# Kernel optimization log

Measured on AMD Instinct MI355X. Metric: run time of the kernel, lower is better.

The kernel has to match this reference:

```python
import jax, jax.numpy as jnp
import numpy as np

N = 100000
E = 1600000


def gcn_conv(x, W, b, src, dst, dinv):
    # PyG GCNConv: h = x @ W; symmetric normalization with self-loops;
    # out[i] = sum_{j->i} dinv[j]*dinv[i]*h[j] + dinv[i]^2*h[i] + b
    h = x @ W
    norm = dinv[src] * dinv[dst]                      # [E]
    msg = h[src] * norm[:, None]                      # [E, d] gather
    out = jax.ops.segment_sum(msg, dst, num_segments=N)  # scatter-add
    out = out + h * (dinv * dinv)[:, None]            # self-loop term
    return out + b


def setup_inputs() -> dict:
    key = jax.random.key(0)
    ks = jax.random.split(key, 8)
    nfeat, nhid, nclass = 128, 128, 40
    x = jax.random.normal(ks[0], (N, nfeat), dtype=jnp.float32)
    edge_index = jax.random.randint(ks[1], (2, E), 0, N, dtype=jnp.int64)
    s = 1.0 / np.sqrt(nfeat)
    W0 = jax.random.uniform(ks[2], (nfeat, nhid), jnp.float32, -s, s)
    b0 = jnp.zeros((nhid,), jnp.float32)
    W1 = jax.random.uniform(ks[3], (nhid, nhid), jnp.float32, -s, s)
    b1 = jnp.zeros((nhid,), jnp.float32)
    W2 = jax.random.uniform(ks[4], (nhid, nclass), jnp.float32, -s, s)
    b2 = jnp.zeros((nclass,), jnp.float32)
    return {"x": x, "W0": W0, "b0": b0, "W1": W1, "b1": b1,
            "W2": W2, "b2": b2, "edge_index": edge_index}


def reference(x, W0, b0, W1, b1, W2, b2, edge_index):
    src, dst = edge_index[0], edge_index[1]
    # degree (with self-loop) on destination nodes, symmetric norm
    deg = jax.ops.segment_sum(jnp.ones((E,), jnp.float32), dst, num_segments=N) + 1.0
    dinv = jax.lax.rsqrt(deg)
    h = gcn_conv(x, W0, b0, src, dst, dinv)
    h = jax.nn.relu(h)  # dropout is identity in eval mode
    h = gcn_conv(h, W1, b1, src, dst, dinv)
    h = jax.nn.relu(h)
    out = gcn_conv(h, W2, b2, src, dst, dinv)
    return out
```

## Files before the change

kernel.cpp:

```cpp
#include <hip/hip_runtime.h>
#include <hip/hip_fp16.h>


#define CAP 8192
#define NBMAX 512

typedef _Float16 f16;
typedef __attribute__((ext_vector_type(8))) _Float16 f16x8;
typedef __attribute__((ext_vector_type(4))) _Float16 f16x4;
typedef __attribute__((ext_vector_type(4))) float f32x4;

__global__ __launch_bounds__(256)
void bucket_prep_kernel(const int* __restrict__ src, const int* __restrict__ dst,
                        int E, int gP1, int NB,
                        int* __restrict__ bucket_cnt, unsigned* __restrict__ bucketbuf,
                        const float* __restrict__ W0, const float* __restrict__ W1,
                        const float* __restrict__ W2,
                        __half* __restrict__ w0t, __half* __restrict__ w1t,
                        __half* __restrict__ w2t) {
  int b = blockIdx.x;
  if (b < gP1) {
    __shared__ int hist[NBMAX];
    __shared__ int cbase[NBMAX];
    int tid = threadIdx.x;
    for (int i = tid; i < NB; i += 256) hist[i] = 0;
    __syncthreads();
    int e0 = b * 4096;
    int eend = min(e0 + 4096, E);
    for (int e = e0 + tid; e < eend; e += 256)
      atomicAdd(&hist[((unsigned)dst[e]) >> 8], 1);
    __syncthreads();
    for (int i = tid; i < NB; i += 256) {
      int h = hist[i];
      cbase[i] = h ? atomicAdd(&bucket_cnt[i], h) : 0;
    }
    __syncthreads();
    for (int i = tid; i < NB; i += 256) hist[i] = 0;
    __syncthreads();
    for (int e = e0 + tid; e < eend; e += 256) {
      int d = dst[e];
      int s = src[e];
      int bk = ((unsigned)d) >> 8;
      int idx = cbase[bk] + atomicAdd(&hist[bk], 1);
      if (idx < CAP)
        bucketbuf[(size_t)bk * CAP + idx] = (((unsigned)s) << 8) | (unsigned)(d & 255);
    }
  } else {
    int i = (b - gP1) * 256 + threadIdx.x;
    if (i < 16384) {
      int n = i >> 7, k = i & 127;
      w0t[i] = __float2half_rn(W0[k * 128 + n]);
    } else if (i < 32768) {
      int j = i - 16384;
      int n = j >> 7, k = j & 127;
      w1t[j] = __float2half_rn(W1[k * 128 + n]);
    } else if (i < 38912) {
      int j = i - 32768;
      int n = j >> 7, k = j & 127;
      w2t[j] = (n < 40) ? __float2half_rn(W2[k * 40 + n]) : __float2half_rn(0.f);
    }
  }
}

struct P2Shared {
  unsigned plist[CAP];
  int cnts[256];
  int sm[256];
};

__device__ __forceinline__
void phase2_body(const unsigned* __restrict__ bucketbuf, const int* __restrict__ bucket_cnt,
                 int* __restrict__ rowptr, float* __restrict__ dinv,
                 int* __restrict__ col, int N, int E, int NB, int b, P2Shared& sh) {
  int tid = threadIdx.x;
  int cnt_b = min(bucket_cnt[b], CAP);

  int part = 0;
  for (int i = tid; i < b; i += 256) part += bucket_cnt[i];
  sh.sm[tid] = part;
  __syncthreads();
#pragma unroll
  for (int off = 128; off > 0; off >>= 1) {
    if (tid < off) sh.sm[tid] += sh.sm[tid + off];
    __syncthreads();
  }
  int base = sh.sm[0];
  __syncthreads();

  for (int i = tid; i < cnt_b; i += 256)
    sh.plist[i] = bucketbuf[(size_t)b * CAP + i];
  sh.cnts[tid] = 0;
  __syncthreads();
  for (int i = tid; i < cnt_b; i += 256)
    atomicAdd(&sh.cnts[sh.plist[i] & 255u], 1);
  __syncthreads();

  int myc = sh.cnts[tid];
  sh.sm[tid] = myc;
  __syncthreads();
#pragma unroll
  for (int off = 1; off < 256; off <<= 1) {
    int u = (tid >= off) ? sh.sm[tid - off] : 0;
    __syncthreads();
    sh.sm[tid] += u;
    __syncthreads();
  }
  int exc = sh.sm[tid] - myc;

  int n = (b << 8) + tid;
  if (n < N) {
    rowptr[n] = base + exc;
    dinv[n] = 1.0f / sqrtf((float)myc + 1.0f);
  }
  if (b == NB - 1 && tid == 0) rowptr[N] = E;
  __syncthreads();

  sh.cnts[tid] = base + exc;
  __syncthreads();
  for (int i = tid; i < cnt_b; i += 256) {
    unsigned p = sh.plist[i];
    int pos = atomicAdd(&sh.cnts[p & 255u], 1);
    col[pos] = (int)(p >> 8);
  }
}

template <typename TIN, bool SCALE>
__device__ __forceinline__
void mfma_gemm128_body(const TIN* __restrict__ X, const __half* __restrict__ Wt,
                       const float* __restrict__ dinv, __half* __restrict__ G,
                       int nrows, int blk, f16 (*xs)[72], f16 (*ws)[72]) {
  const int tid = threadIdx.x;
  const int wave = tid >> 6;
  const int lane = tid & 63;
  const int mrow = lane & 15;
  const int kg = lane >> 4;
  const int row0 = blk * 128;

  f32x4 acc[2][8];
#pragma unroll
  for (int i = 0; i < 2; ++i)
#pragma unroll
    for (int j = 0; j < 8; ++j) acc[i][j] = (f32x4){0.f, 0.f, 0.f, 0.f};

  for (int k0 = 0; k0 < 128; k0 += 64) {
    if constexpr (sizeof(TIN) == 4) {
#pragma unroll
      for (int t = tid; t < 2048; t += 256) {
        int r = t >> 4;
        int kk = (t & 15) * 4;
        float4 v = make_float4(0.f, 0.f, 0.f, 0.f);
        if (row0 + r < nrows)
          v = *(const float4*)((const float*)X + (size_t)(row0 + r) * 128 + k0 + kk);
        f16x4 hv = {(f16)v.x, (f16)v.y, (f16)v.z, (f16)v.w};
        *(f16x4*)&xs[r][kk] = hv;
      }
    } else {
#pragma unroll
      for (int t = tid; t < 1024; t += 256) {
        int r = t >> 3;
        int kk = (t & 7) * 8;
        f16x8 v = (f16x8){0, 0, 0, 0, 0, 0, 0, 0};
        if (row0 + r < nrows)
          v = *(const f16x8*)((const f16*)X + (size_t)(row0 + r) * 128 + k0 + kk);
        *(f16x8*)&xs[r][kk] = v;
      }
    }
#pragma unroll
    for (int t = tid; t < 1024; t += 256) {
      int r = t >> 3;
      int kk = (t & 7) * 8;
      *(f16x8*)&ws[r][kk] =
          *(const f16x8*)((const f16*)Wt + (size_t)r * 128 + k0 + kk);
    }
    __syncthreads();
#pragma unroll
    for (int ks = 0; ks < 64; ks += 32) {
      f16x8 a0 = *(const f16x8*)&xs[wave * 32 + mrow][ks + kg * 8];
      f16x8 a1 = *(const f16x8*)&xs[wave * 32 + 16 + mrow][ks + kg * 8];
#pragma unroll
      for (int nt = 0; nt < 8; ++nt) {
        f16x8 b = *(const f16x8*)&ws[nt * 16 + mrow][ks + kg * 8];
        acc[0][nt] = __builtin_amdgcn_mfma_f32_16x16x32_f16(a0, b, acc[0][nt], 0, 0, 0);
        acc[1][nt] = __builtin_amdgcn_mfma_f32_16x16x32_f16(a1, b, acc[1][nt], 0, 0, 0);
      }
    }
    __syncthreads();
  }
#pragma unroll
  for (int mt = 0; mt < 2; ++mt) {
    int rbase = row0 + wave * 32 + mt * 16 + kg * 4;
#pragma unroll
    for (int i = 0; i < 4; ++i) {
      int grow = rbase + i;
      if (grow < nrows) {
        float s = SCALE ? dinv[grow] : 1.0f;
        __half* gp = G + (size_t)grow * 128 + mrow;
#pragma unroll
        for (int nt = 0; nt < 8; ++nt)
          gp[nt * 16] = __float2half_rn(s * acc[mt][nt][i]);
      }
    }
  }
}

__global__ __launch_bounds__(256)
void mfma_gemm128_kernel(const __half* __restrict__ X, const __half* __restrict__ Wt,
                         const float* __restrict__ dinv, __half* __restrict__ G,
                         int nrows) {
  __shared__ f16 xs[128][72];
  __shared__ f16 ws[128][72];
  mfma_gemm128_body<__half, true>(X, Wt, dinv, G, nrows, blockIdx.x, xs, ws);
}

__global__ __launch_bounds__(256)
void gemm128_build_kernel(const float* __restrict__ X, const __half* __restrict__ Wt,
                          __half* __restrict__ G, int nrows, int gGemm,
                          const unsigned* __restrict__ bucketbuf,
                          const int* __restrict__ bucket_cnt,
                          int* __restrict__ rowptr, float* __restrict__ dinv,
                          int* __restrict__ col, int N, int E, int NB) {
  __shared__ char shraw[2 * 128 * 72 * sizeof(f16)];
  if ((int)blockIdx.x < gGemm) {
    f16 (*xs)[72] = (f16(*)[72])shraw;
    f16 (*ws)[72] = (f16(*)[72])(shraw + 128 * 72 * sizeof(f16));
    mfma_gemm128_body<float, false>(X, Wt, nullptr, G, nrows, blockIdx.x, xs, ws);
  } else {
    phase2_body(bucketbuf, bucket_cnt, rowptr, dinv, col, N, E, NB,
                blockIdx.x - gGemm, *(P2Shared*)shraw);
  }
}

__global__ __launch_bounds__(256)
void mfma_gemm48_kernel(const __half* __restrict__ X, const __half* __restrict__ Wt,
                        const float* __restrict__ dinv, __half* __restrict__ G,
                        int nrows) {
  __shared__ f16 xs[128][72];
  __shared__ f16 ws[48][72];
  const int tid = threadIdx.x;
  const int wave = tid >> 6;
  const int lane = tid & 63;
  const int mrow = lane & 15;
  const int kg = lane >> 4;
  const int row0 = blockIdx.x * 128;

  f32x4 acc[2][3];
#pragma unroll
  for (int i = 0; i < 2; ++i)
#pragma unroll
    for (int j = 0; j < 3; ++j) acc[i][j] = (f32x4){0.f, 0.f, 0.f, 0.f};

  for (int k0 = 0; k0 < 128; k0 += 64) {
#pragma unroll
    for (int t = tid; t < 1024; t += 256) {
      int r = t >> 3;
      int kk = (t & 7) * 8;
      f16x8 v = (f16x8){0, 0, 0, 0, 0, 0, 0, 0};
      if (row0 + r < nrows)
        v = *(const f16x8*)((const f16*)X + (size_t)(row0 + r) * 128 + k0 + kk);
      *(f16x8*)&xs[r][kk] = v;
    }
#pragma unroll
    for (int t = tid; t < 384; t += 256) {
      int r = t >> 3;
      int kk = (t & 7) * 8;
      *(f16x8*)&ws[r][kk] =
          *(const f16x8*)((const f16*)Wt + (size_t)r * 128 + k0 + kk);
    }
    __syncthreads();
#pragma unroll
    for (int ks = 0; ks < 64; ks += 32) {
      f16x8 a0 = *(const f16x8*)&xs[wave * 32 + mrow][ks + kg * 8];
      f16x8 a1 = *(const f16x8*)&xs[wave * 32 + 16 + mrow][ks + kg * 8];
#pragma unroll
      for (int nt = 0; nt < 3; ++nt) {
        f16x8 b = *(const f16x8*)&ws[nt * 16 + mrow][ks + kg * 8];
        acc[0][nt] = __builtin_amdgcn_mfma_f32_16x16x32_f16(a0, b, acc[0][nt], 0, 0, 0);
        acc[1][nt] = __builtin_amdgcn_mfma_f32_16x16x32_f16(a1, b, acc[1][nt], 0, 0, 0);
      }
    }
    __syncthreads();
  }
#pragma unroll
  for (int mt = 0; mt < 2; ++mt) {
    int rbase = row0 + wave * 32 + mt * 16 + kg * 4;
#pragma unroll
    for (int i = 0; i < 4; ++i) {
      int grow = rbase + i;
      if (grow < nrows) {
        float s = dinv[grow];
#pragma unroll
        for (int nt = 0; nt < 3; ++nt) {
          int c = nt * 16 + mrow;
          if (c < 40)
            G[(size_t)grow * 40 + c] = __float2half_rn(s * acc[mt][nt][i]);
        }
      }
    }
  }
}

template <bool RELU, bool WEIGHTED, typename TOUT>
__global__ __launch_bounds__(256)
void aggregate128_kernel(const __half* __restrict__ G, const int* __restrict__ rowptr,
                         const int* __restrict__ col, const float* __restrict__ dinv,
                         const float* __restrict__ bias, TOUT* __restrict__ out,
                         int n, int Em1) {
  int wid = threadIdx.x >> 6;
  int lane = threadIdx.x & 63;
  int node = blockIdx.x * 4 + wid;
  if (node >= n) return;

  int sub = lane >> 4;
  int c = lane & 15;
  const float4* g4 = (const float4*)G;

  int e = rowptr[node];
  int end = rowptr[node + 1];
  float di = dinv[node];

  float a0 = 0.f, a1 = 0.f, a2 = 0.f, a3 = 0.f,
        a4 = 0.f, a5 = 0.f, a6 = 0.f, a7 = 0.f;

  auto accumw = [&](float4 raw, float w) {
    const __half2* h = (const __half2*)&raw;
    float2 f0 = __half22float2(h[0]);
    float2 f1 = __half22float2(h[1]);
    float2 f2 = __half22float2(h[2]);
    float2 f3 = __half22float2(h[3]);
    a0 = fmaf(w, f0.x, a0); a1 = fmaf(w, f0.y, a1);
    a2 = fmaf(w, f1.x, a2); a3 = fmaf(w, f1.y, a3);
    a4 = fmaf(w, f2.x, a4); a5 = fmaf(w, f2.y, a5);
    a6 = fmaf(w, f3.x, a6); a7 = fmaf(w, f3.y, a7);
  };

  if (sub == 0)
    accumw(g4[(size_t)node * 16 + c], WEIGHTED ? di : 1.0f);

  int base = e;
  int i0 = base + sub * 4;
  int s0 = col[min(i0, Em1)];
  int s1 = col[min(i0 + 1, Em1)];
  int s2 = col[min(i0 + 2, Em1)];
  int s3 = col[min(i0 + 3, Em1)];

  while (base < end) {
    int ii = base + sub * 4;
    float4 z = make_float4(0.f, 0.f, 0.f, 0.f);
    float4 r0 = z, r1 = z, r2 = z, r3 = z;
    if (ii < end)     r0 = g4[(size_t)s0 * 16 + c];
    if (ii + 1 < end) r1 = g4[(size_t)s1 * 16 + c];
    if (ii + 2 < end) r2 = g4[(size_t)s2 * 16 + c];
    if (ii + 3 < end) r3 = g4[(size_t)s3 * 16 + c];
    float w0 = 1.f, w1 = 1.f, w2 = 1.f, w3 = 1.f;
    if (WEIGHTED) { w0 = dinv[s0]; w1 = dinv[s1]; w2 = dinv[s2]; w3 = dinv[s3]; }
    base += 16;
    int ni = base + sub * 4;
    int t0 = col[min(ni, Em1)];
    int t1 = col[min(ni + 1, Em1)];
    int t2 = col[min(ni + 2, Em1)];
    int t3 = col[min(ni + 3, Em1)];
    accumw(r0, w0);
    accumw(r1, w1);
    accumw(r2, w2);
    accumw(r3, w3);
    s0 = t0; s1 = t1; s2 = t2; s3 = t3;
  }

  a0 += __shfl_xor(a0, 16); a1 += __shfl_xor(a1, 16);
  a2 += __shfl_xor(a2, 16); a3 += __shfl_xor(a3, 16);
  a4 += __shfl_xor(a4, 16); a5 += __shfl_xor(a5, 16);
  a6 += __shfl_xor(a6, 16); a7 += __shfl_xor(a7, 16);
  a0 += __shfl_xor(a0, 32); a1 += __shfl_xor(a1, 32);
  a2 += __shfl_xor(a2, 32); a3 += __shfl_xor(a3, 32);
  a4 += __shfl_xor(a4, 32); a5 += __shfl_xor(a5, 32);
  a6 += __shfl_xor(a6, 32); a7 += __shfl_xor(a7, 32);

  if (sub == 0) {
    const float4* b4 = (const float4*)bias;
    float4 bb0 = b4[c * 2];
    float4 bb1 = b4[c * 2 + 1];
    float o[8] = {di * a0 + bb0.x, di * a1 + bb0.y, di * a2 + bb0.z,
                  di * a3 + bb0.w, di * a4 + bb1.x, di * a5 + bb1.y,
                  di * a6 + bb1.z, di * a7 + bb1.w};
    if (RELU) {
#pragma unroll
      for (int j = 0; j < 8; ++j) o[j] = fmaxf(o[j], 0.f);
    }
    if constexpr (sizeof(TOUT) == 2) {
      union { __half2 h[4]; float4 f; } u;
      u.h[0] = __floats2half2_rn(o[0], o[1]);
      u.h[1] = __floats2half2_rn(o[2], o[3]);
      u.h[2] = __floats2half2_rn(o[4], o[5]);
      u.h[3] = __floats2half2_rn(o[6], o[7]);
      *(float4*)((__half*)out + (size_t)node * 128 + c * 8) = u.f;
    } else {
      float4* op = (float4*)((float*)out + (size_t)node * 128 + c * 8);
      op[0] = make_float4(o[0], o[1], o[2], o[3]);
      op[1] = make_float4(o[4], o[5], o[6], o[7]);
    }
  }
}

__global__ __launch_bounds__(256)
void aggregate40_kernel(const __half* __restrict__ G, const int* __restrict__ rowptr,
                        const int* __restrict__ col, const float* __restrict__ dinv,
                        const float* __restrict__ bias, float* __restrict__ out,
                        int n, int Em1) {
  int wid = threadIdx.x >> 6;
  int lane = threadIdx.x & 63;
  int node = blockIdx.x * 4 + wid;
  if (node >= n) return;

  int sub = lane / 10;
  int c = lane % 10;
  bool act = sub < 6;
  const float2* g2 = (const float2*)G;

  int e = rowptr[node];
  int end = rowptr[node + 1];
  float di = dinv[node];

  float ax = 0.f, ay = 0.f, az = 0.f, aw = 0.f;
  auto acc2 = [&](float2 raw) {
    float2 f0 = __half22float2(*(const __half2*)&raw.x);
    float2 f1 = __half22float2(*(const __half2*)&raw.y);
    ax += f0.x; ay += f0.y; az += f1.x; aw += f1.y;
  };
  if (lane < 10) acc2(g2[(size_t)node * 10 + c]);

  int base = e;
  int i0 = base + sub * 2;
  int s0 = col[min(i0, Em1)];
  int s1 = col[min(i0 + 1, Em1)];

  while (base < end) {
    int ii = base + sub * 2;
    float2 z = make_float2(0.f, 0.f);
    float2 r0 = z, r1 = z;
    if (act && ii < end)     r0 = g2[(size_t)s0 * 10 + c];
    if (act && ii + 1 < end) r1 = g2[(size_t)s1 * 10 + c];
    base += 12;
    int ni = base + sub * 2;
    int t0 = col[min(ni, Em1)];
    int t1 = col[min(ni + 1, Em1)];
    acc2(r0);
    acc2(r1);
    s0 = t0; s1 = t1;
  }

  float bx = __shfl(ax, lane + 30), by = __shfl(ay, lane + 30),
        bz = __shfl(az, lane + 30), bw = __shfl(aw, lane + 30);
  ax += bx; ay += by; az += bz; aw += bw;
  float c1x = __shfl(ax, lane + 10), c1y = __shfl(ay, lane + 10),
        c1z = __shfl(az, lane + 10), c1w = __shfl(aw, lane + 10);
  float c2x = __shfl(ax, lane + 20), c2y = __shfl(ay, lane + 20),
        c2z = __shfl(az, lane + 20), c2w = __shfl(aw, lane + 20);

  if (lane < 10) {
    float sx = ax + c1x + c2x;
    float sy = ay + c1y + c2y;
    float sz = az + c1z + c2z;
    float sw = aw + c1w + c2w;
    float4 bb = ((const float4*)bias)[c];
    float4 o = make_float4(di * sx + bb.x, di * sy + bb.y, di * sz + bb.z,
                           di * sw + bb.w);
    ((float4*)out)[(size_t)node * 10 + c] = o;
  }
}

extern "C" void kernel_launch(void* const* d_in, const int* in_sizes, int n_in,
                              void* d_out, int out_size, void* d_ws, size_t ws_size,
                              hipStream_t stream) {
  const float* x = (const float*)d_in[0];
  const float* W0 = (const float*)d_in[1];
  const float* b0 = (const float*)d_in[2];
  const float* W1 = (const float*)d_in[3];
  const float* b1 = (const float*)d_in[4];
  const float* W2 = (const float*)d_in[5];
  const float* b2 = (const float*)d_in[6];
  const int* ei = (const int*)d_in[7];

  const int N = in_sizes[0] / 128;
  const int E = in_sizes[7] / 2;
  const int* src = ei;
  const int* dst = ei + E;
  const int NB = (N + 255) >> 8;

  char* w = (char*)d_ws;
  size_t off = 0;
  auto alloc = [&](size_t bytes) -> void* {
    void* p = w + off;
    off = (off + bytes + 255) & ~(size_t)255;
    return p;
  };
  int* bucket_cnt = (int*)alloc((size_t)NBMAX * 4);
  float* dinv = (float*)alloc((size_t)N * 4);
  int* rowptr = (int*)alloc((size_t)(N + 1) * 4);
  int* col = (int*)alloc((size_t)E * 4);
  unsigned* bucketbuf = (unsigned*)alloc((size_t)NB * CAP * 4);
  __half* gbuf = (__half*)alloc((size_t)N * 128 * 2);
  __half* hbuf = (__half*)alloc((size_t)N * 128 * 2);
  __half* w0t = (__half*)alloc(128 * 128 * 2);
  __half* w1t = (__half*)alloc(128 * 128 * 2);
  __half* w2t = (__half*)alloc(48 * 128 * 2);
  (void)ws_size;

  hipMemsetAsync(bucket_cnt, 0, (size_t)NBMAX * 4, stream);

  dim3 blk(256);
  int gP1 = (E + 4095) / 4096;
  int gW = (38912 + 255) / 256;
  int gGemm = (N + 127) / 128;
  int gAgg = (N + 3) / 4;

  bucket_prep_kernel<<<gP1 + gW, blk, 0, stream>>>(src, dst, E, gP1, NB,
                                                   bucket_cnt, bucketbuf,
                                                   W0, W1, W2, w0t, w1t, w2t);
  gemm128_build_kernel<<<gGemm + NB, blk, 0, stream>>>(x, w0t, gbuf, N, gGemm,
                                                       bucketbuf, bucket_cnt,
                                                       rowptr, dinv, col, N, E, NB);

  aggregate128_kernel<true, true, __half><<<gAgg, blk, 0, stream>>>(
      gbuf, rowptr, col, dinv, b0, hbuf, N, E - 1);
  mfma_gemm128_kernel<<<gGemm, blk, 0, stream>>>(hbuf, w1t, dinv, gbuf, N);
  aggregate128_kernel<true, false, __half><<<gAgg, blk, 0, stream>>>(
      gbuf, rowptr, col, dinv, b1, hbuf, N, E - 1);
  mfma_gemm48_kernel<<<gGemm, blk, 0, stream>>>(hbuf, w2t, dinv, gbuf, N);
  aggregate40_kernel<<<gAgg, blk, 0, stream>>>(gbuf, rowptr, col, dinv, b2,
                                               (float*)d_out, N, E - 1);
}
```

Measured before the change: 365.0 us.

## Process four nodes per wave with software-pipelined column-index prefetch in aggregation

Each wavefront in the aggregation kernels now handles four consecutive nodes instead of one. While gathering the current node's neighbors, it prefetches the next node's rowptr and column indices. The first 20 (or 24) edges are gathered unconditionally with zeroed weights for out-of-range slots, and a tail loop handles the rest. This hides index-load latency and amortizes launch and wave setup, at the cost of fewer waves in flight and some wasted gathers for low-degree nodes.

```diff
diff --git a/kernel.cpp b/kernel.cpp
--- a/kernel.cpp
+++ b/kernel.cpp
@@ -304,100 +304,124 @@
 void aggregate128_kernel(const __half* __restrict__ G, const int* __restrict__ rowptr,
                          const int* __restrict__ col, const float* __restrict__ dinv,
                          const float* __restrict__ bias, TOUT* __restrict__ out,
-                         int n, int Em1) {
+                         int n) {
+  constexpr int NPW = 4;
   int wid = threadIdx.x >> 6;
   int lane = threadIdx.x & 63;
-  int node = blockIdx.x * 4 + wid;
-  if (node >= n) return;
+  int n0 = (blockIdx.x * 4 + wid) * NPW;
+  if (n0 >= n) return;
 
   int sub = lane >> 4;
   int c = lane & 15;
   const float4* g4 = (const float4*)G;
 
-  int e = rowptr[node];
-  int end = rowptr[node + 1];
-  float di = dinv[node];
-
-  float a0 = 0.f, a1 = 0.f, a2 = 0.f, a3 = 0.f,
-        a4 = 0.f, a5 = 0.f, a6 = 0.f, a7 = 0.f;
-
-  auto accumw = [&](float4 raw, float w) {
-    const __half2* h = (const __half2*)&raw;
-    float2 f0 = __half22float2(h[0]);
-    float2 f1 = __half22float2(h[1]);
-    float2 f2 = __half22float2(h[2]);
-    float2 f3 = __half22float2(h[3]);
-    a0 = fmaf(w, f0.x, a0); a1 = fmaf(w, f0.y, a1);
-    a2 = fmaf(w, f1.x, a2); a3 = fmaf(w, f1.y, a3);
-    a4 = fmaf(w, f2.x, a4); a5 = fmaf(w, f2.y, a5);
-    a6 = fmaf(w, f3.x, a6); a7 = fmaf(w, f3.y, a7);
-  };
-
-  if (sub == 0)
-    accumw(g4[(size_t)node * 16 + c], WEIGHTED ? di : 1.0f);
-
-  int base = e;
-  int i0 = base + sub * 4;
-  int s0 = col[min(i0, Em1)];
-  int s1 = col[min(i0 + 1, Em1)];
-  int s2 = col[min(i0 + 2, Em1)];
-  int s3 = col[min(i0 + 3, Em1)];
-
-  while (base < end) {
-    int ii = base + sub * 4;
-    float4 z = make_float4(0.f, 0.f, 0.f, 0.f);
-    float4 r0 = z, r1 = z, r2 = z, r3 = z;
-    if (ii < end)     r0 = g4[(size_t)s0 * 16 + c];
-    if (ii + 1 < end) r1 = g4[(size_t)s1 * 16 + c];
-    if (ii + 2 < end) r2 = g4[(size_t)s2 * 16 + c];
-    if (ii + 3 < end) r3 = g4[(size_t)s3 * 16 + c];
-    float w0 = 1.f, w1 = 1.f, w2 = 1.f, w3 = 1.f;
-    if (WEIGHTED) { w0 = dinv[s0]; w1 = dinv[s1]; w2 = dinv[s2]; w3 = dinv[s3]; }
-    base += 16;
-    int ni = base + sub * 4;
-    int t0 = col[min(ni, Em1)];
-    int t1 = col[min(ni + 1, Em1)];
-    int t2 = col[min(ni + 2, Em1)];
-    int t3 = col[min(ni + 3, Em1)];
-    accumw(r0, w0);
-    accumw(r1, w1);
-    accumw(r2, w2);
-    accumw(r3, w3);
-    s0 = t0; s1 = t1; s2 = t2; s3 = t3;
-  }
-
-  a0 += __shfl_xor(a0, 16); a1 += __shfl_xor(a1, 16);
-  a2 += __shfl_xor(a2, 16); a3 += __shfl_xor(a3, 16);
-  a4 += __shfl_xor(a4, 16); a5 += __shfl_xor(a5, 16);
-  a6 += __shfl_xor(a6, 16); a7 += __shfl_xor(a7, 16);
-  a0 += __shfl_xor(a0, 32); a1 += __shfl_xor(a1, 32);
-  a2 += __shfl_xor(a2, 32); a3 += __shfl_xor(a3, 32);
-  a4 += __shfl_xor(a4, 32); a5 += __shfl_xor(a5, 32);
-  a6 += __shfl_xor(a6, 32); a7 += __shfl_xor(a7, 32);
-
-  if (sub == 0) {
-    const float4* b4 = (const float4*)bias;
-    float4 bb0 = b4[c * 2];
-    float4 bb1 = b4[c * 2 + 1];
-    float o[8] = {di * a0 + bb0.x, di * a1 + bb0.y, di * a2 + bb0.z,
-                  di * a3 + bb0.w, di * a4 + bb1.x, di * a5 + bb1.y,
-                  di * a6 + bb1.z, di * a7 + bb1.w};
-    if (RELU) {
-#pragma unroll
-      for (int j = 0; j < 8; ++j) o[j] = fmaxf(o[j], 0.f);
-    }
-    if constexpr (sizeof(TOUT) == 2) {
-      union { __half2 h[4]; float4 f; } u;
-      u.h[0] = __floats2half2_rn(o[0], o[1]);
-      u.h[1] = __floats2half2_rn(o[2], o[3]);
-      u.h[2] = __floats2half2_rn(o[4], o[5]);
-      u.h[3] = __floats2half2_rn(o[6], o[7]);
-      *(float4*)((__half*)out + (size_t)node * 128 + c * 8) = u.f;
-    } else {
-      float4* op = (float4*)((float*)out + (size_t)node * 128 + c * 8);
-      op[0] = make_float4(o[0], o[1], o[2], o[3]);
-      op[1] = make_float4(o[4], o[5], o[6], o[7]);
-    }
+  int eA = rowptr[n0], endA = rowptr[n0 + 1];
+  int n1 = min(n0 + 1, n - 1);
+  int eB = rowptr[n1], endB = rowptr[n1 + 1];
+
+  int lastA = (endA > eA) ? endA - 1 : 0;
+  int iA = eA + sub;
+  int cA0 = col[min(iA,      lastA)];
+  int cA1 = col[min(iA + 4,  lastA)];
+  int cA2 = col[min(iA + 8,  lastA)];
+  int cA3 = col[min(iA + 12, lastA)];
+  int cA4 = col[min(iA + 16, lastA)];
+
+#pragma unroll
+  for (int j = 0; j < NPW; ++j) {
+    int node = n0 + j;
+    if (node >= n) break;
+
+    float4 r0 = g4[(size_t)cA0 * 16 + c];
+    float4 r1 = g4[(size_t)cA1 * 16 + c];
+    float4 r2 = g4[(size_t)cA2 * 16 + c];
+    float4 r3 = g4[(size_t)cA3 * 16 + c];
+    float4 r4 = g4[(size_t)cA4 * 16 + c];
+    float4 rs = g4[(size_t)node * 16 + c];
+    float dv0 = 1.f, dv1 = 1.f, dv2 = 1.f, dv3 = 1.f, dv4 = 1.f;
+    if (WEIGHTED) {
+      dv0 = dinv[cA0]; dv1 = dinv[cA1]; dv2 = dinv[cA2];
+      dv3 = dinv[cA3]; dv4 = dinv[cA4];
+    }
+    float di = dinv[node];
+
+    int n2 = min(node + 2, n - 1);
+    int eC = rowptr[n2];
+    int endC = rowptr[n2 + 1];
+
+    int lastB = (endB > eB) ? endB - 1 : 0;
+    int iB = eB + sub;
+    int cB0 = col[min(iB,      lastB)];
+    int cB1 = col[min(iB + 4,  lastB)];
+    int cB2 = col[min(iB + 8,  lastB)];
+    int cB3 = col[min(iB + 12, lastB)];
+    int cB4 = col[min(iB + 16, lastB)];
+
+    float a0 = 0.f, a1 = 0.f, a2 = 0.f, a3 = 0.f,
+          a4 = 0.f, a5 = 0.f, a6 = 0.f, a7 = 0.f;
+    auto accumw = [&](float4 raw, float w) {
+      const __half2* h = (const __half2*)&raw;
+      float2 f0 = __half22float2(h[0]);
+      float2 f1 = __half22float2(h[1]);
+      float2 f2 = __half22float2(h[2]);
+      float2 f3 = __half22float2(h[3]);
+      a0 = fmaf(w, f0.x, a0); a1 = fmaf(w, f0.y, a1);
+      a2 = fmaf(w, f1.x, a2); a3 = fmaf(w, f1.y, a3);
+      a4 = fmaf(w, f2.x, a4); a5 = fmaf(w, f2.y, a5);
+      a6 = fmaf(w, f3.x, a6); a7 = fmaf(w, f3.y, a7);
+    };
+    accumw(rs, (sub == 0) ? (WEIGHTED ? di : 1.f) : 0.f);
+    accumw(r0, (iA      < endA) ? dv0 : 0.f);
+    accumw(r1, (iA + 4  < endA) ? dv1 : 0.f);
+    accumw(r2, (iA + 8  < endA) ? dv2 : 0.f);
+    accumw(r3, (iA + 12 < endA) ? dv3 : 0.f);
+    accumw(r4, (iA + 16 < endA) ? dv4 : 0.f);
+
+    for (int t = eA + 20; t < endA; t += 4) {
+      int it = t + sub;
+      if (it < endA) {
+        int sc = col[it];
+        accumw(g4[(size_t)sc * 16 + c], WEIGHTED ? dinv[sc] : 1.f);
+      }
+    }
+
+    a0 += __shfl_xor(a0, 16); a1 += __shfl_xor(a1, 16);
+    a2 += __shfl_xor(a2, 16); a3 += __shfl_xor(a3, 16);
+    a4 += __shfl_xor(a4, 16); a5 += __shfl_xor(a5, 16);
+    a6 += __shfl_xor(a6, 16); a7 += __shfl_xor(a7, 16);
+    a0 += __shfl_xor(a0, 32); a1 += __shfl_xor(a1, 32);
+    a2 += __shfl_xor(a2, 32); a3 += __shfl_xor(a3, 32);
+    a4 += __shfl_xor(a4, 32); a5 += __shfl_xor(a5, 32);
+    a6 += __shfl_xor(a6, 32); a7 += __shfl_xor(a7, 32);
+
+    if (sub == 0) {
+      const float4* b4 = (const float4*)bias;
+      float4 bb0 = b4[c * 2];
+      float4 bb1 = b4[c * 2 + 1];
+      float o[8] = {di * a0 + bb0.x, di * a1 + bb0.y, di * a2 + bb0.z,
+                    di * a3 + bb0.w, di * a4 + bb1.x, di * a5 + bb1.y,
+                    di * a6 + bb1.z, di * a7 + bb1.w};
+      if (RELU) {
+#pragma unroll
+        for (int k = 0; k < 8; ++k) o[k] = fmaxf(o[k], 0.f);
+      }
+      if constexpr (sizeof(TOUT) == 2) {
+        union { __half2 h[4]; float4 f; } u;
+        u.h[0] = __floats2half2_rn(o[0], o[1]);
+        u.h[1] = __floats2half2_rn(o[2], o[3]);
+        u.h[2] = __floats2half2_rn(o[4], o[5]);
+        u.h[3] = __floats2half2_rn(o[6], o[7]);
+        *(float4*)((__half*)out + (size_t)node * 128 + c * 8) = u.f;
+      } else {
+        float4* op = (float4*)((float*)out + (size_t)node * 128 + c * 8);
+        op[0] = make_float4(o[0], o[1], o[2], o[3]);
+        op[1] = make_float4(o[4], o[5], o[6], o[7]);
+      }
+    }
+
+    eA = eB; endA = endB; eB = eC; endB = endC;
+    iA = eA + sub;
+    cA0 = cB0; cA1 = cB1; cA2 = cB2; cA3 = cB3; cA4 = cB4;
   }
 }
 
@@ -405,66 +429,95 @@
 void aggregate40_kernel(const __half* __restrict__ G, const int* __restrict__ rowptr,
                         const int* __restrict__ col, const float* __restrict__ dinv,
                         const float* __restrict__ bias, float* __restrict__ out,
-                        int n, int Em1) {
+                        int n) {
+  constexpr int NPW = 4;
   int wid = threadIdx.x >> 6;
   int lane = threadIdx.x & 63;
-  int node = blockIdx.x * 4 + wid;
-  if (node >= n) return;
+  int n0 = (blockIdx.x * 4 + wid) * NPW;
+  if (n0 >= n) return;
 
   int sub = lane / 10;
   int c = lane % 10;
   bool act = sub < 6;
   const float2* g2 = (const float2*)G;
 
-  int e = rowptr[node];
-  int end = rowptr[node + 1];
-  float di = dinv[node];
-
-  float ax = 0.f, ay = 0.f, az = 0.f, aw = 0.f;
-  auto acc2 = [&](float2 raw) {
-    float2 f0 = __half22float2(*(const __half2*)&raw.x);
-    float2 f1 = __half22float2(*(const __half2*)&raw.y);
-    ax += f0.x; ay += f0.y; az += f1.x; aw += f1.y;
-  };
-  if (lane < 10) acc2(g2[(size_t)node * 10 + c]);
-
-  int base = e;
-  int i0 = base + sub * 2;
-  int s0 = col[min(i0, Em1)];
-  int s1 = col[min(i0 + 1, Em1)];
-
-  while (base < end) {
-    int ii = base + sub * 2;
-    float2 z = make_float2(0.f, 0.f);
-    float2 r0 = z, r1 = z;
-    if (act && ii < end)     r0 = g2[(size_t)s0 * 10 + c];
-    if (act && ii + 1 < end) r1 = g2[(size_t)s1 * 10 + c];
-    base += 12;
-    int ni = base + sub * 2;
-    int t0 = col[min(ni, Em1)];
-    int t1 = col[min(ni + 1, Em1)];
-    acc2(r0);
-    acc2(r1);
-    s0 = t0; s1 = t1;
-  }
-
-  float bx = __shfl(ax, lane + 30), by = __shfl(ay, lane + 30),
-        bz = __shfl(az, lane + 30), bw = __shfl(aw, lane + 30);
-  ax += bx; ay += by; az += bz; aw += bw;
-  float c1x = __shfl(ax, lane + 10), c1y = __shfl(ay, lane + 10),
-        c1z = __shfl(az, lane + 10), c1w = __shfl(aw, lane + 10);
-  float c2x = __shfl(ax, lane + 20), c2y = __shfl(ay, lane + 20),
-        c2z = __shfl(az, lane + 20), c2w = __shfl(aw, lane + 20);
-
-  if (lane < 10) {
-    float sx = ax + c1x + c2x;
-    float sy = ay + c1y + c2y;
-    float sz = az + c1z + c2z;
-    float sw = aw + c1w + c2w;
-    float4 bb = ((const float4*)bias)[c];
-    float4 o = make_float4(di * sx + bb.x, di * sy + bb.y, di * sz + bb.z,
-                           di * sw + bb.w);
-    ((float4*)out)[(size_t)node * 10 + c] = o;
+  int eA = rowptr[n0], endA = rowptr[n0 + 1];
+  int n1 = min(n0 + 1, n - 1);
+  int eB = rowptr[n1], endB = rowptr[n1 + 1];
+
+  int lastA = (endA > eA) ? endA - 1 : 0;
+  int iA = eA + sub * 4;
+  int cA0 = col[min(iA,     lastA)];
+  int cA1 = col[min(iA + 1, lastA)];
+  int cA2 = col[min(iA + 2, lastA)];
+  int cA3 = col[min(iA + 3, lastA)];
+
+#pragma unroll
+  for (int j = 0; j < NPW; ++j) {
+    int node = n0 + j;
+    if (node >= n) break;
+
+    float2 r0 = g2[(size_t)cA0 * 10 + c];
+    float2 r1 = g2[(size_t)cA1 * 10 + c];
+    float2 r2 = g2[(size_t)cA2 * 10 + c];
+    float2 r3 = g2[(size_t)cA3 * 10 + c];
+    float2 rs = g2[(size_t)node * 10 + c];
+    float di = dinv[node];
+
+    int n2 = min(node + 2, n - 1);
+    int eC = rowptr[n2];
+    int endC = rowptr[n2 + 1];
+
+    int lastB = (endB > eB) ? endB - 1 : 0;
+    int iB = eB + sub * 4;
+    int cB0 = col[min(iB,     lastB)];
+    int cB1 = col[min(iB + 1, lastB)];
+    int cB2 = col[min(iB + 2, lastB)];
+    int cB3 = col[min(iB + 3, lastB)];
+
+    float ax = 0.f, ay = 0.f, az = 0.f, aw = 0.f;
+    auto acc2w = [&](float2 raw, float w) {
+      float2 f0 = __half22float2(*(const __half2*)&raw.x);
+      float2 f1 = __half22float2(*(const __half2*)&raw.y);
+      ax = fmaf(w, f0.x, ax); ay = fmaf(w, f0.y, ay);
+      az = fmaf(w, f1.x, az); aw = fmaf(w, f1.y, aw);
+    };
+    acc2w(rs, (lane < 10) ? 1.f : 0.f);
+    acc2w(r0, (act && iA     < endA) ? 1.f : 0.f);
+    acc2w(r1, (act && iA + 1 < endA) ? 1.f : 0.f);
+    acc2w(r2, (act && iA + 2 < endA) ? 1.f : 0.f);
+    acc2w(r3, (act && iA + 3 < endA) ? 1.f : 0.f);
+
+    for (int t = eA + 24; t < endA; t += 6) {
+      int it = t + sub;
+      if (act && it < endA) {
+        int sc = col[it];
+        acc2w(g2[(size_t)sc * 10 + c], 1.f);
+      }
+    }
+
+    float bx = __shfl(ax, lane + 30), by = __shfl(ay, lane + 30),
+          bz = __shfl(az, lane + 30), bw = __shfl(aw, lane + 30);
+    ax += bx; ay += by; az += bz; aw += bw;
+    float c1x = __shfl(ax, lane + 10), c1y = __shfl(ay, lane + 10),
+          c1z = __shfl(az, lane + 10), c1w = __shfl(aw, lane + 10);
+    float c2x = __shfl(ax, lane + 20), c2y = __shfl(ay, lane + 20),
+          c2z = __shfl(az, lane + 20), c2w = __shfl(aw, lane + 20);
+
+    if (lane < 10) {
+      float sx = ax + c1x + c2x;
+      float sy = ay + c1y + c2y;
+      float sz = az + c1z + c2z;
+      float sw = aw + c1w + c2w;
+      float4 bb = ((const float4*)bias)[c];
+      float4 o = make_float4(di * sx + bb.x, di * sy + bb.y, di * sz + bb.z,
+                             di * sw + bb.w);
+      ((float4*)out)[(size_t)node * 10 + c] = o;
+    }
+
+    eA = eB; endA = endB; eB = eC; endB = endC;
+    iA = eA + sub * 4;
+    cA0 = cB0; cA1 = cB1; cA2 = cB2; cA3 = cB3;
   }
 }
 
@@ -511,7 +564,7 @@
   int gP1 = (E + 4095) / 4096;
   int gW = (38912 + 255) / 256;
   int gGemm = (N + 127) / 128;
-  int gAgg = (N + 3) / 4;
+  int gAgg = (N + 15) / 16;
 
   bucket_prep_kernel<<<gP1 + gW, blk, 0, stream>>>(src, dst, E, gP1, NB,
                                                    bucket_cnt, bucketbuf,
@@ -521,11 +574,11 @@
                                                        rowptr, dinv, col, N, E, NB);
 
   aggregate128_kernel<true, true, __half><<<gAgg, blk, 0, stream>>>(
-      gbuf, rowptr, col, dinv, b0, hbuf, N, E - 1);
+      gbuf, rowptr, col, dinv, b0, hbuf, N);
   mfma_gemm128_kernel<<<gGemm, blk, 0, stream>>>(hbuf, w1t, dinv, gbuf, N);
   aggregate128_kernel<true, false, __half><<<gAgg, blk, 0, stream>>>(
-      gbuf, rowptr, col, dinv, b1, hbuf, N, E - 1);
+      gbuf, rowptr, col, dinv, b1, hbuf, N);
   mfma_gemm48_kernel<<<gGemm, blk, 0, stream>>>(hbuf, w2t, dinv, gbuf, N);
   aggregate40_kernel<<<gAgg, blk, 0, stream>>>(gbuf, rowptr, col, dinv, b2,
-                                               (float*)d_out, N, E - 1);
-}
+                                               (float*)d_out, N);
+}
```

Result: faster. 342.8 us (-6.1%).
